# Kernel optimization log

Measured on AMD Instinct MI355X. Metric: run time of the kernel, lower is better.

The kernel has to match this reference:

```python
import jax, jax.numpy as jnp
import numpy as np

B, S, D, H, DFF = 2, 2048, 512, 8, 2048
DH = D // H
EPS = 1e-5


def setup_inputs() -> dict:
    key = jax.random.key(0)
    ks = jax.random.split(key, 12)
    g = lambda k, shape, s=0.02: jax.random.normal(k, shape, dtype=jnp.float32) * s
    x = jax.random.normal(ks[0], (B, S, D), dtype=jnp.float32)
    # additive causal mask: 0 on/below diag, -inf above
    neg = jnp.finfo(jnp.float32).min
    attn_mask = jnp.where(jnp.tril(jnp.ones((S, S), dtype=bool)), 0.0, neg).astype(jnp.float32)
    return {
        "x": x,
        "attn_mask": attn_mask,
        "Wq": g(ks[1], (D, D)), "bq": jnp.zeros((D,), jnp.float32),
        "Wk": g(ks[2], (D, D)), "bk": jnp.zeros((D,), jnp.float32),
        "Wv": g(ks[3], (D, D)), "bv": jnp.zeros((D,), jnp.float32),
        "Wo": g(ks[4], (D, D)), "bo": jnp.zeros((D,), jnp.float32),
        "head_alphas": jnp.ones((H,), jnp.float32),
        "ln1_g": jnp.ones((D,), jnp.float32), "ln1_b": jnp.zeros((D,), jnp.float32),
        "W1": g(ks[5], (DFF, D)), "b1": jnp.zeros((DFF,), jnp.float32),
        "W2": g(ks[6], (D, DFF)), "b2": jnp.zeros((D,), jnp.float32),
        "ln2_g": jnp.ones((D,), jnp.float32), "ln2_b": jnp.zeros((D,), jnp.float32),
    }


def _layer_norm(h, g, b):
    mu = jnp.mean(h, axis=-1, keepdims=True)
    var = jnp.mean((h - mu) ** 2, axis=-1, keepdims=True)
    return (h - mu) * jax.lax.rsqrt(var + EPS) * g + b


def reference(x, attn_mask, Wq, bq, Wk, bk, Wv, bv, Wo, bo, head_alphas,
              ln1_g, ln1_b, W1, b1, W2, b2, ln2_g, ln2_b):
    scale = jnp.sqrt(jnp.asarray(DH, dtype=x.dtype))
    # projections (torch Linear: x @ W.T + b)
    q = (x @ Wq.T + bq).reshape(B, S, H, DH).transpose(0, 2, 1, 3)  # bhsd
    k = (x @ Wk.T + bk).reshape(B, S, H, DH).transpose(0, 2, 1, 3)
    v = (x @ Wv.T + bv).reshape(B, S, H, DH).transpose(0, 2, 1, 3)
    attn = jnp.einsum('bhqd,bhkd->bhqk', q, k) / scale
    attn = attn + attn_mask  # broadcast [S,S] over batch/heads
    attn = jax.nn.softmax(attn, axis=-1)
    ctx = jnp.einsum('bhqk,bhkd->bhqd', attn, v)
    ctx = ctx * head_alphas[None, :, None, None]
    ctx = ctx.transpose(0, 2, 1, 3).reshape(B, S, D)
    attn_out = ctx @ Wo.T + bo
    # residual + LN
    h = _layer_norm(x + attn_out, ln1_g, ln1_b)
    # FFN (linear -> ReLU -> linear), residual + LN
    ff = jax.nn.relu(h @ W1.T + b1) @ W2.T + b2
    out = _layer_norm(h + ff, ln2_g, ln2_b)
    return out
```

## Files before the change

### kernel.cpp

```cpp
#include <hip/hip_runtime.h>
#include <hip/hip_bf16.h>
#include <math.h>

#define BB 2
#define SS 2048
#define DD 512
#define HH 8
#define DH 64
#define DFF 2048
#define MM (BB*SS)
#define EPS 1e-5f

typedef __attribute__((ext_vector_type(8))) short bf16x8;
typedef __attribute__((ext_vector_type(4))) float f32x4;

#define GL2LDS(g, l)                                                        \
    __builtin_amdgcn_global_load_lds(                                       \
        (const __attribute__((address_space(1))) void*)(unsigned long long)(g), \
        (__attribute__((address_space(3))) void*)(unsigned int)(unsigned long long)(l), \
        16, 0, 0)

struct Cvt7 {
    const float* s[7];
    unsigned short* d[7];
    unsigned off[8];
};

__global__ __launch_bounds__(256) void cvt_k(Cvt7 a)
{
    unsigned i = blockIdx.x * 256 + threadIdx.x;
    int seg = 0;
    #pragma unroll
    for (int t = 1; t < 7; ++t) seg += (i >= a.off[t]);
    unsigned li = i - a.off[seg];
    float4 v = ((const float4*)a.s[seg])[li];
    union { __hip_bfloat16 h[4]; uint2 u; } t;
    t.h[0] = __float2bfloat16(v.x);
    t.h[1] = __float2bfloat16(v.y);
    t.h[2] = __float2bfloat16(v.z);
    t.h[3] = __float2bfloat16(v.w);
    ((uint2*)a.d[seg])[li] = t.u;
}

template<int TM, int TN>
static __device__ __forceinline__ void gemm_core(
    __hip_bfloat16* As, __hip_bfloat16* Bs,
    const __hip_bfloat16* __restrict__ A, const __hip_bfloat16* __restrict__ Bw,
    const float* __restrict__ bias, const float* __restrict__ resid,
    void* __restrict__ Cout, int N_, int K_, int mode, float oscale)
{
    const int tid   = threadIdx.x;
    const int w     = tid >> 6;
    const int lane  = tid & 63;
    const int quad  = lane >> 4;
    const int col16 = lane & 15;
    const int m0 = blockIdx.y * TM;
    const int n0 = blockIdx.x * TN;
    constexpr int MI = TM / 32;
    constexpr int NJ = TN / 32;
    const int wm = (w >> 1) * (TM / 2);
    const int wn = (w & 1) * (TN / 2);

    const int srow = lane >> 3;
    const int scol = (lane & 7) * 8;
    constexpr int CH_A  = TM / 8;
    constexpr int CH_T  = (TM + TN) / 8;
    constexpr int TPW   = CH_T / 4;

    f32x4 acc[MI][NJ] = {};

    for (int k0 = 0; k0 < K_; k0 += 64) {
        __syncthreads();
        #pragma unroll
        for (int t = 0; t < TPW; ++t) {
            const int c = w * TPW + t;
            if (c < CH_A) {
                GL2LDS(A  + (size_t)(m0 + c*8 + srow) * K_ + k0 + scol,
                       (char*)As + c * 1024);
            } else {
                const int cb = c - CH_A;
                GL2LDS(Bw + (size_t)(n0 + cb*8 + srow) * K_ + k0 + scol,
                       (char*)Bs + cb * 1024);
            }
        }
        __syncthreads();

        #pragma unroll
        for (int kk = 0; kk < 64; kk += 32) {
            bf16x8 af[MI], bf[NJ];
            #pragma unroll
            for (int i = 0; i < MI; ++i)
                af[i] = *(const bf16x8*)(As + (wm + i*16 + col16) * 64 + kk + quad*8);
            #pragma unroll
            for (int j = 0; j < NJ; ++j)
                bf[j] = *(const bf16x8*)(Bs + (wn + j*16 + col16) * 64 + kk + quad*8);
            #pragma unroll
            for (int i = 0; i < MI; ++i)
                #pragma unroll
                for (int j = 0; j < NJ; ++j)
                    acc[i][j] = __builtin_amdgcn_mfma_f32_16x16x32_bf16(
                        af[i], bf[j], acc[i][j], 0, 0, 0);
        }
    }

    #pragma unroll
    for (int i = 0; i < MI; ++i) {
        #pragma unroll
        for (int r = 0; r < 4; ++r) {
            const int m = m0 + wm + i*16 + quad*4 + r;
            #pragma unroll
            for (int j = 0; j < NJ; ++j) {
                const int n = n0 + wn + j*16 + col16;
                float vv = acc[i][j][r] + bias[n];
                if (mode == 0) {
                    size_t idx = (size_t)m * N_ + n;
                    float* Cf = (float*)Cout;
                    if (resid) vv += resid[idx];
                    Cf[idx] = vv;
                } else if (mode == 3) {
                    ((__hip_bfloat16*)Cout)[(size_t)m * N_ + n] =
                        __float2bfloat16(fmaxf(vv, 0.f));
                } else {
                    const int b = m >> 11, s = m & (SS - 1);
                    const int hh = n >> 6, d = n & (DH - 1);
                    if (mode == 1)
                        ((__hip_bfloat16*)Cout)[(((size_t)(b*HH + hh))*SS + s)*DH + d] =
                            __float2bfloat16(vv * oscale);
                    else
                        ((__hip_bfloat16*)Cout)[(((size_t)(b*HH + hh))*DH + d)*SS + s] =
                            __float2bfloat16(vv);
                }
            }
        }
    }
}

__global__ __launch_bounds__(256) void gemm128_k(
    const __hip_bfloat16* __restrict__ A, const __hip_bfloat16* __restrict__ Bw,
    const float* __restrict__ bias, const float* __restrict__ resid,
    void* __restrict__ Cout, int N_, int K_, int mode, float oscale)
{
    __shared__ __hip_bfloat16 As[128*64];
    __shared__ __hip_bfloat16 Bs[128*64];
    gemm_core<128,128>(As, Bs, A, Bw, bias, resid, Cout, N_, K_, mode, oscale);
}

__global__ __launch_bounds__(256) void gemm64_k(
    const __hip_bfloat16* __restrict__ A, const __hip_bfloat16* __restrict__ Bw,
    const float* __restrict__ bias, const float* __restrict__ resid,
    void* __restrict__ Cout, int N_, int K_, int mode, float oscale)
{
    __shared__ __hip_bfloat16 As[64*64];
    __shared__ __hip_bfloat16 Bs[64*64];
    gemm_core<64,64>(As, Bs, A, Bw, bias, resid, Cout, N_, K_, mode, oscale);
}

__global__ __launch_bounds__(256) void qkv_fused_k(
    const __hip_bfloat16* __restrict__ A, const __hip_bfloat16* __restrict__ Wqkv,
    const float* __restrict__ bq, const float* __restrict__ bk,
    const float* __restrict__ bv,
    __hip_bfloat16* __restrict__ qb, __hip_bfloat16* __restrict__ kb,
    __hip_bfloat16* __restrict__ vtb)
{
    __shared__ __hip_bfloat16 As[128*64];
    __shared__ __hip_bfloat16 Bs[128*64];
    const int tid   = threadIdx.x;
    const int w     = tid >> 6;
    const int lane  = tid & 63;
    const int quad  = lane >> 4;
    const int col16 = lane & 15;
    const int m0 = blockIdx.y * 128;
    const int n0 = blockIdx.x * 128;
    const int wm = (w >> 1) * 64;
    const int wn = (w & 1) * 64;
    const int srow = lane >> 3;
    const int scol = (lane & 7) * 8;

    f32x4 acc[4][4] = {};

    for (int k0 = 0; k0 < DD; k0 += 64) {
        __syncthreads();
        #pragma unroll
        for (int t = 0; t < 8; ++t) {
            const int c = w * 8 + t;
            if (c < 16) {
                GL2LDS(A    + (size_t)(m0 + c*8 + srow) * DD + k0 + scol,
                       (char*)As + c * 1024);
            } else {
                const int cb = c - 16;
                GL2LDS(Wqkv + (size_t)(n0 + cb*8 + srow) * DD + k0 + scol,
                       (char*)Bs + cb * 1024);
            }
        }
        __syncthreads();

        #pragma unroll
        for (int kk = 0; kk < 64; kk += 32) {
            bf16x8 af[4], bf[4];
            #pragma unroll
            for (int i = 0; i < 4; ++i)
                af[i] = *(const bf16x8*)(As + (wm + i*16 + col16) * 64 + kk + quad*8);
            #pragma unroll
            for (int j = 0; j < 4; ++j)
                bf[j] = *(const bf16x8*)(Bs + (wn + j*16 + col16) * 64 + kk + quad*8);
            #pragma unroll
            for (int i = 0; i < 4; ++i)
                #pragma unroll
                for (int j = 0; j < 4; ++j)
                    acc[i][j] = __builtin_amdgcn_mfma_f32_16x16x32_bf16(
                        af[i], bf[j], acc[i][j], 0, 0, 0);
        }
    }

    const int z = n0 >> 9;
    const float* bias = (z == 0) ? bq : (z == 1) ? bk : bv;
    __hip_bfloat16* dst = (z == 0) ? qb : (z == 1) ? kb : vtb;
    const float sc = (z == 0) ? 0.125f : 1.0f;
    #pragma unroll
    for (int i = 0; i < 4; ++i) {
        #pragma unroll
        for (int r = 0; r < 4; ++r) {
            const int m = m0 + wm + i*16 + quad*4 + r;
            const int b = m >> 11, s = m & (SS - 1);
            #pragma unroll
            for (int j = 0; j < 4; ++j) {
                const int n  = n0 + wn + j*16 + col16;
                const int nn = n & 511;
                const int hh = nn >> 6, d = nn & (DH - 1);
                float vv = (acc[i][j][r] + bias[nn]) * sc;
                if (z < 2)
                    dst[(((size_t)(b*HH + hh))*SS + s)*DH + d] = __float2bfloat16(vv);
                else
                    dst[(((size_t)(b*HH + hh))*DH + d)*SS + s] = __float2bfloat16(vv);
            }
        }
    }
}

__global__ __launch_bounds__(256) void attn_mfma_k(
    const __hip_bfloat16* __restrict__ Q,
    const __hip_bfloat16* __restrict__ K,
    const __hip_bfloat16* __restrict__ VT,
    const float* __restrict__ halpha,
    __hip_bfloat16* __restrict__ ctx)
{
    const int w    = threadIdx.x >> 6;
    const int lane = threadIdx.x & 63;
    const int quad = lane >> 4;
    const int col  = lane & 15;
    const int xl   = blockIdx.x;
    const int bh   = ((xl & 7) << 1) | (xl >> 3);
    const int b    = bh >> 3, h = bh & 7;
    const int qt   = gridDim.y - 1 - blockIdx.y;
    const int q0   = qt * 16;
    const int cd   = q0 >> 6;
    const int nchunk = cd + 1;

    const __hip_bfloat16* Qbh = Q  + (size_t)bh * SS * DH;
    const __hip_bfloat16* Kbh = K  + (size_t)bh * SS * DH;
    const __hip_bfloat16* Vbh = VT + (size_t)bh * DH * SS;

    __shared__ __hip_bfloat16 p_lds[4][2][64][8];
    __shared__ float o_lds[4][16][68];
    __shared__ float l_lds[4][16];

    bf16x8 qf0 = *(const bf16x8*)(Qbh + (size_t)(q0 + col) * DH + quad * 8);
    bf16x8 qf1 = *(const bf16x8*)(Qbh + (size_t)(q0 + col) * DH + 32 + quad * 8);

    f32x4 acc_o[4] = {};
    float lp[4] = {0.f, 0.f, 0.f, 0.f};

    for (int c = w; c < nchunk; c += 4) {
        const int k0 = c * 64;

        f32x4 sacc[4];
        #pragma unroll
        for (int ks = 0; ks < 4; ++ks) {
            const __hip_bfloat16* kp = Kbh + (size_t)(k0 + ks*16 + col) * DH + quad * 8;
            bf16x8 kb0 = *(const bf16x8*)(kp);
            bf16x8 kb1 = *(const bf16x8*)(kp + 32);
            f32x4 z = {};
            z = __builtin_amdgcn_mfma_f32_16x16x32_bf16(qf0, kb0, z, 0, 0, 0);
            z = __builtin_amdgcn_mfma_f32_16x16x32_bf16(qf1, kb1, z, 0, 0, 0);
            sacc[ks] = z;
        }

        float pv[4][4];
        if (c == cd) {
            #pragma unroll
            for (int ks = 0; ks < 4; ++ks) {
                int kg = k0 + ks*16 + col;
                #pragma unroll
                for (int r = 0; r < 4; ++r) {
                    int qg = q0 + quad*4 + r;
                    pv[ks][r] = (kg > qg) ? 0.f : __expf(sacc[ks][r]);
                }
            }
        } else {
            #pragma unroll
            for (int ks = 0; ks < 4; ++ks)
                #pragma unroll
                for (int r = 0; r < 4; ++r)
                    pv[ks][r] = __expf(sacc[ks][r]);
        }
        #pragma unroll
        for (int r = 0; r < 4; ++r)
            lp[r] += (pv[0][r] + pv[1][r]) + (pv[2][r] + pv[3][r]);

        #pragma unroll
        for (int ks = 0; ks < 4; ++ks) {
            int keyl = ks*16 + col;
            int kh = keyl >> 5;
            int lr = ((keyl >> 3) & 3) * 16;
            int j  = keyl & 7;
            #pragma unroll
            for (int r = 0; r < 4; ++r)
                p_lds[w][kh][lr + quad*4 + r][j] = __float2bfloat16(pv[ks][r]);
        }

        bf16x8 pa0 = *(const bf16x8*)&p_lds[w][0][lane][0];
        bf16x8 pa1 = *(const bf16x8*)&p_lds[w][1][lane][0];
        #pragma unroll
        for (int d = 0; d < 4; ++d) {
            const __hip_bfloat16* vp = Vbh + (size_t)(d*16 + col) * SS + k0 + quad * 8;
            bf16x8 vb0 = *(const bf16x8*)(vp);
            bf16x8 vb1 = *(const bf16x8*)(vp + 32);
            acc_o[d] = __builtin_amdgcn_mfma_f32_16x16x32_bf16(pa0, vb0, acc_o[d], 0, 0, 0);
            acc_o[d] = __builtin_amdgcn_mfma_f32_16x16x32_bf16(pa1, vb1, acc_o[d], 0, 0, 0);
        }
    }

    #pragma unroll
    for (int r = 0; r < 4; ++r) {
        float s_ = lp[r];
        #pragma unroll
        for (int o = 1; o < 16; o <<= 1) s_ += __shfl_xor(s_, o);
        lp[r] = s_;
    }

    if (col == 0) {
        #pragma unroll
        for (int r = 0; r < 4; ++r) l_lds[w][quad*4 + r] = lp[r];
    }
    #pragma unroll
    for (int d = 0; d < 4; ++d)
        #pragma unroll
        for (int r = 0; r < 4; ++r)
            o_lds[w][quad*4 + r][d*16 + col] = acc_o[d][r];
    __syncthreads();

    const float ha = halpha[h];
    #pragma unroll
    for (int r = 0; r < 4; ++r) {
        const int row = quad*4 + r;
        float L = (l_lds[0][row] + l_lds[1][row]) + (l_lds[2][row] + l_lds[3][row]);
        float val = (o_lds[0][row][w*16+col] + o_lds[1][row][w*16+col])
                  + (o_lds[2][row][w*16+col] + o_lds[3][row][w*16+col]);
        ctx[((size_t)(b*SS + q0 + row))*DD + h*64 + w*16 + col] =
            __float2bfloat16(val * ha / L);
    }
}

__global__ __launch_bounds__(256) void ln_k(
    const float* __restrict__ in, const float* __restrict__ g,
    const float* __restrict__ bta, float* __restrict__ out,
    __hip_bfloat16* __restrict__ outb)
{
    const int row = blockIdx.x;
    const float* p = in + (size_t)row * DD;
    const int t = threadIdx.x;
    float v0 = p[t], v1 = p[t + 256];
    __shared__ float red[256];
    red[t] = v0 + v1;
    __syncthreads();
    for (int o = 128; o > 0; o >>= 1) { if (t < o) red[t] += red[t + o]; __syncthreads(); }
    float mu = red[0] * (1.f / DD);
    __syncthreads();
    float d0 = v0 - mu, d1 = v1 - mu;
    red[t] = d0*d0 + d1*d1;
    __syncthreads();
    for (int o = 128; o > 0; o >>= 1) { if (t < o) red[t] += red[t + o]; __syncthreads(); }
    float rstd = rsqrtf(red[0] * (1.f / DD) + EPS);
    float o0 = d0 * rstd * g[t]       + bta[t];
    float o1 = d1 * rstd * g[t + 256] + bta[t + 256];
    out[(size_t)row * DD + t]       = o0;
    out[(size_t)row * DD + t + 256] = o1;
    if (outb) {
        outb[(size_t)row * DD + t]       = __float2bfloat16(o0);
        outb[(size_t)row * DD + t + 256] = __float2bfloat16(o1);
    }
}

extern "C" void kernel_launch(void* const* d_in, const int* in_sizes, int n_in,
                              void* d_out, int out_size, void* d_ws, size_t ws_size,
                              hipStream_t stream)
{
    const float* x    = (const float*)d_in[0];
    const float* Wq   = (const float*)d_in[2];
    const float* bq   = (const float*)d_in[3];
    const float* Wk   = (const float*)d_in[4];
    const float* bk   = (const float*)d_in[5];
    const float* Wv   = (const float*)d_in[6];
    const float* bv   = (const float*)d_in[7];
    const float* Wo   = (const float*)d_in[8];
    const float* bo   = (const float*)d_in[9];
    const float* hal  = (const float*)d_in[10];
    const float* ln1g = (const float*)d_in[11];
    const float* ln1b = (const float*)d_in[12];
    const float* W1   = (const float*)d_in[13];
    const float* b1   = (const float*)d_in[14];
    const float* W2   = (const float*)d_in[15];
    const float* b2   = (const float*)d_in[16];
    const float* ln2g = (const float*)d_in[17];
    const float* ln2b = (const float*)d_in[18];
    float* out = (float*)d_out;

    char* ws = (char*)d_ws;
    const size_t MB = 1ull << 20;
    __hip_bfloat16* Wqb = (__hip_bfloat16*)(ws);
    __hip_bfloat16* Wkb = (__hip_bfloat16*)(ws + MB/2);
    __hip_bfloat16* Wvb = (__hip_bfloat16*)(ws + MB);
    __hip_bfloat16* Wob = (__hip_bfloat16*)(ws + MB + MB/2);
    __hip_bfloat16* W1b = (__hip_bfloat16*)(ws + 2*MB);
    __hip_bfloat16* W2b = (__hip_bfloat16*)(ws + 4*MB);
    __hip_bfloat16* xb  = (__hip_bfloat16*)(ws + 6*MB);
    __hip_bfloat16* qb  = (__hip_bfloat16*)(ws + 10*MB);
    __hip_bfloat16* kb  = (__hip_bfloat16*)(ws + 14*MB);
    __hip_bfloat16* vtb = (__hip_bfloat16*)(ws + 18*MB);
    __hip_bfloat16* ctxb= (__hip_bfloat16*)(ws + 22*MB);
    float* h1  = (float*)(ws + 26*MB);
    float* h   = (float*)(ws + 34*MB);
    __hip_bfloat16* hb  = (__hip_bfloat16*)(ws + 42*MB);
    __hip_bfloat16* ff1b= (__hip_bfloat16*)(ws + 10*MB);
    float* f2  = (float*)(ws + 26*MB);

    dim3 blk(256);

    Cvt7 ca;
    ca.s[0] = x;  ca.d[0] = (unsigned short*)xb;
    ca.s[1] = Wq; ca.d[1] = (unsigned short*)Wqb;
    ca.s[2] = Wk; ca.d[2] = (unsigned short*)Wkb;
    ca.s[3] = Wv; ca.d[3] = (unsigned short*)Wvb;
    ca.s[4] = Wo; ca.d[4] = (unsigned short*)Wob;
    ca.s[5] = W1; ca.d[5] = (unsigned short*)W1b;
    ca.s[6] = W2; ca.d[6] = (unsigned short*)W2b;
    unsigned offs[8] = {0, 524288, 589824, 655360, 720896, 786432, 1048576, 1310720};
    for (int i = 0; i < 8; ++i) ca.off[i] = offs[i];
    cvt_k<<<dim3(5120), blk, 0, stream>>>(ca);

    qkv_fused_k<<<dim3((3*DD)/128, MM/128), blk, 0, stream>>>(
        xb, Wqb, bq, bk, bv, qb, kb, vtb);

    attn_mfma_k<<<dim3(BB*HH, SS/16), blk, 0, stream>>>(qb, kb, vtb, hal, ctxb);

    gemm64_k<<<dim3(DD/64, MM/64), blk, 0, stream>>>(
        ctxb, Wob, bo, x, h1, DD, DD, 0, 1.0f);
    ln_k<<<dim3(MM), blk, 0, stream>>>(h1, ln1g, ln1b, h, hb);

    gemm128_k<<<dim3(DFF/128, MM/128), blk, 0, stream>>>(
        hb, W1b, b1, nullptr, ff1b, DFF, DD, 3, 1.0f);
    gemm64_k<<<dim3(DD/64, MM/64), blk, 0, stream>>>(
        ff1b, W2b, b2, h, f2, DD, DFF, 0, 1.0f);
    ln_k<<<dim3(MM), blk, 0, stream>>>(f2, ln2g, ln2b, out, nullptr);
}
```

Before: 280.0 us.

## Enlarge attention query tile to 64 rows per block for K/V reuse

Each attention block now processes 64 query rows (four 16-row MFMA tiles) instead of 16, so every K and V fragment loaded from global memory is reused across four query tiles. The grid shrinks fourfold and the block-index swizzle is dropped. The cost is more registers per thread (4x4 accumulators plus Q fragments) and a larger shared-memory buffer, which may lower occupancy. Causal-load balance also gets coarser with fewer, longer blocks.

```diff
diff --git a/kernel.cpp b/kernel.cpp
--- a/kernel.cpp
+++ b/kernel.cpp
@@ -248,115 +248,121 @@
     const int lane = threadIdx.x & 63;
     const int quad = lane >> 4;
     const int col  = lane & 15;
-    const int xl   = blockIdx.x;
-    const int bh   = ((xl & 7) << 1) | (xl >> 3);
+    const int bh   = blockIdx.x;
     const int b    = bh >> 3, h = bh & 7;
     const int qt   = gridDim.y - 1 - blockIdx.y;
-    const int q0   = qt * 16;
-    const int cd   = q0 >> 6;
-    const int nchunk = cd + 1;
+    const int q0   = qt * 64;
+    const int nchunk = qt + 1;
 
     const __hip_bfloat16* Qbh = Q  + (size_t)bh * SS * DH;
     const __hip_bfloat16* Kbh = K  + (size_t)bh * SS * DH;
     const __hip_bfloat16* Vbh = VT + (size_t)bh * DH * SS;
 
-    __shared__ __hip_bfloat16 p_lds[4][2][64][8];
-    __shared__ float o_lds[4][16][68];
-    __shared__ float l_lds[4][16];
-
-    bf16x8 qf0 = *(const bf16x8*)(Qbh + (size_t)(q0 + col) * DH + quad * 8);
-    bf16x8 qf1 = *(const bf16x8*)(Qbh + (size_t)(q0 + col) * DH + 32 + quad * 8);
-
-    f32x4 acc_o[4] = {};
-    float lp[4] = {0.f, 0.f, 0.f, 0.f};
+    __shared__ float smem[16640];
+    __hip_bfloat16* p_base = (__hip_bfloat16*)smem + (size_t)w * 4096;
+    float* lbuf = smem + 4 * 4096;
+
+    bf16x8 qf[4][2];
+    #pragma unroll
+    for (int mi = 0; mi < 4; ++mi) {
+        const __hip_bfloat16* qp = Qbh + (size_t)(q0 + mi*16 + col) * DH + quad * 8;
+        qf[mi][0] = *(const bf16x8*)(qp);
+        qf[mi][1] = *(const bf16x8*)(qp + 32);
+    }
+
+    f32x4 acc_o[4][4] = {};
+    float lp[4][4] = {};
 
     for (int c = w; c < nchunk; c += 4) {
         const int k0 = c * 64;
-
-        f32x4 sacc[4];
+        const bool diag = (c == qt);
+
         #pragma unroll
         for (int ks = 0; ks < 4; ++ks) {
             const __hip_bfloat16* kp = Kbh + (size_t)(k0 + ks*16 + col) * DH + quad * 8;
             bf16x8 kb0 = *(const bf16x8*)(kp);
             bf16x8 kb1 = *(const bf16x8*)(kp + 32);
-            f32x4 z = {};
-            z = __builtin_amdgcn_mfma_f32_16x16x32_bf16(qf0, kb0, z, 0, 0, 0);
-            z = __builtin_amdgcn_mfma_f32_16x16x32_bf16(qf1, kb1, z, 0, 0, 0);
-            sacc[ks] = z;
-        }
-
-        float pv[4][4];
-        if (c == cd) {
-            #pragma unroll
-            for (int ks = 0; ks < 4; ++ks) {
-                int kg = k0 + ks*16 + col;
+            const int keyl = ks*16 + col;
+            const int kh = keyl >> 5;
+            const int lr = ((keyl >> 3) & 3) * 16;
+            const int j  = keyl & 7;
+            const int kg = k0 + keyl;
+            #pragma unroll
+            for (int mi = 0; mi < 4; ++mi) {
+                f32x4 s = {};
+                s = __builtin_amdgcn_mfma_f32_16x16x32_bf16(qf[mi][0], kb0, s, 0, 0, 0);
+                s = __builtin_amdgcn_mfma_f32_16x16x32_bf16(qf[mi][1], kb1, s, 0, 0, 0);
                 #pragma unroll
                 for (int r = 0; r < 4; ++r) {
-                    int qg = q0 + quad*4 + r;
-                    pv[ks][r] = (kg > qg) ? 0.f : __expf(sacc[ks][r]);
+                    float p;
+                    if (diag) {
+                        int qg = q0 + mi*16 + quad*4 + r;
+                        p = (kg > qg) ? 0.f : __expf(s[r]);
+                    } else {
+                        p = __expf(s[r]);
+                    }
+                    lp[mi][r] += p;
+                    p_base[mi*1024 + kh*512 + (lr + quad*4 + r)*8 + j] =
+                        __float2bfloat16(p);
                 }
             }
-        } else {
-            #pragma unroll
-            for (int ks = 0; ks < 4; ++ks)
-                #pragma unroll
-                for (int r = 0; r < 4; ++r)
-                    pv[ks][r] = __expf(sacc[ks][r]);
-        }
-        #pragma unroll
-        for (int r = 0; r < 4; ++r)
-            lp[r] += (pv[0][r] + pv[1][r]) + (pv[2][r] + pv[3][r]);
-
-        #pragma unroll
-        for (int ks = 0; ks < 4; ++ks) {
-            int keyl = ks*16 + col;
-            int kh = keyl >> 5;
-            int lr = ((keyl >> 3) & 3) * 16;
-            int j  = keyl & 7;
-            #pragma unroll
-            for (int r = 0; r < 4; ++r)
-                p_lds[w][kh][lr + quad*4 + r][j] = __float2bfloat16(pv[ks][r]);
-        }
-
-        bf16x8 pa0 = *(const bf16x8*)&p_lds[w][0][lane][0];
-        bf16x8 pa1 = *(const bf16x8*)&p_lds[w][1][lane][0];
+        }
+
+        bf16x8 pa[4][2];
+        #pragma unroll
+        for (int mi = 0; mi < 4; ++mi) {
+            pa[mi][0] = *(const bf16x8*)(p_base + mi*1024 + lane*8);
+            pa[mi][1] = *(const bf16x8*)(p_base + mi*1024 + 512 + lane*8);
+        }
         #pragma unroll
         for (int d = 0; d < 4; ++d) {
             const __hip_bfloat16* vp = Vbh + (size_t)(d*16 + col) * SS + k0 + quad * 8;
             bf16x8 vb0 = *(const bf16x8*)(vp);
             bf16x8 vb1 = *(const bf16x8*)(vp + 32);
-            acc_o[d] = __builtin_amdgcn_mfma_f32_16x16x32_bf16(pa0, vb0, acc_o[d], 0, 0, 0);
-            acc_o[d] = __builtin_amdgcn_mfma_f32_16x16x32_bf16(pa1, vb1, acc_o[d], 0, 0, 0);
-        }
-    }
-
-    #pragma unroll
-    for (int r = 0; r < 4; ++r) {
-        float s_ = lp[r];
-        #pragma unroll
-        for (int o = 1; o < 16; o <<= 1) s_ += __shfl_xor(s_, o);
-        lp[r] = s_;
-    }
-
+            #pragma unroll
+            for (int mi = 0; mi < 4; ++mi) {
+                acc_o[mi][d] = __builtin_amdgcn_mfma_f32_16x16x32_bf16(pa[mi][0], vb0, acc_o[mi][d], 0, 0, 0);
+                acc_o[mi][d] = __builtin_amdgcn_mfma_f32_16x16x32_bf16(pa[mi][1], vb1, acc_o[mi][d], 0, 0, 0);
+            }
+        }
+    }
+
+    #pragma unroll
+    for (int mi = 0; mi < 4; ++mi)
+        #pragma unroll
+        for (int r = 0; r < 4; ++r) {
+            float s_ = lp[mi][r];
+            #pragma unroll
+            for (int o = 1; o < 16; o <<= 1) s_ += __shfl_xor(s_, o);
+            lp[mi][r] = s_;
+        }
+
+    __syncthreads();
+    float* obuf = smem + (size_t)w * 4096;
+    #pragma unroll
+    for (int mi = 0; mi < 4; ++mi)
+        #pragma unroll
+        for (int d = 0; d < 4; ++d)
+            #pragma unroll
+            for (int r = 0; r < 4; ++r)
+                obuf[(mi*16 + quad*4 + r)*64 + d*16 + col] = acc_o[mi][d][r];
     if (col == 0) {
         #pragma unroll
-        for (int r = 0; r < 4; ++r) l_lds[w][quad*4 + r] = lp[r];
-    }
-    #pragma unroll
-    for (int d = 0; d < 4; ++d)
-        #pragma unroll
-        for (int r = 0; r < 4; ++r)
-            o_lds[w][quad*4 + r][d*16 + col] = acc_o[d][r];
+        for (int mi = 0; mi < 4; ++mi)
+            #pragma unroll
+            for (int r = 0; r < 4; ++r)
+                lbuf[w*64 + mi*16 + quad*4 + r] = lp[mi][r];
+    }
     __syncthreads();
 
     const float ha = halpha[h];
     #pragma unroll
-    for (int r = 0; r < 4; ++r) {
-        const int row = quad*4 + r;
-        float L = (l_lds[0][row] + l_lds[1][row]) + (l_lds[2][row] + l_lds[3][row]);
-        float val = (o_lds[0][row][w*16+col] + o_lds[1][row][w*16+col])
-                  + (o_lds[2][row][w*16+col] + o_lds[3][row][w*16+col]);
-        ctx[((size_t)(b*SS + q0 + row))*DD + h*64 + w*16 + col] =
+    for (int rr = 0; rr < 16; ++rr) {
+        const int row = w*16 + rr;
+        float L = (lbuf[row] + lbuf[64 + row]) + (lbuf[128 + row] + lbuf[192 + row]);
+        float val = (smem[row*64 + lane] + smem[4096 + row*64 + lane])
+                  + (smem[8192 + row*64 + lane] + smem[12288 + row*64 + lane]);
+        ctx[((size_t)(b*SS + q0 + row))*DD + h*64 + lane] =
             __float2bfloat16(val * ha / L);
     }
 }
@@ -451,7 +457,7 @@
     qkv_fused_k<<<dim3((3*DD)/128, MM/128), blk, 0, stream>>>(
         xb, Wqb, bq, bk, bv, qb, kb, vtb);
 
-    attn_mfma_k<<<dim3(BB*HH, SS/16), blk, 0, stream>>>(qb, kb, vtb, hal, ctxb);
+    attn_mfma_k<<<dim3(BB*HH, SS/64), blk, 0, stream>>>(qb, kb, vtb, hal, ctxb);
 
     gemm64_k<<<dim3(DD/64, MM/64), blk, 0, stream>>>(
         ctxb, Wob, bo, x, h1, DD, DD, 0, 1.0f);
```

Measured after the change: 263.8 us. 5.8% less time.
